# Kernel tuning notes

Measured on AMD Instinct MI355X. Metric: run time of the kernel, lower is better.

Reference implementation:

```python
import jax, jax.numpy as jnp
import numpy as np


def setup_inputs() -> dict:
    key = jax.random.key(0)
    ks = jax.random.split(key, 4)
    B, H, W, C = 4, 64, 64, 64
    d = C // 8
    s = 0.05
    return {
        "x": jax.random.normal(ks[0], (B, H, W, C), dtype=jnp.float32),
        "Wq": jax.random.normal(ks[1], (C, d), dtype=jnp.float32) * s,
        "bq": jnp.zeros((d,), dtype=jnp.float32),
        "Wk": jax.random.normal(ks[2], (C, d), dtype=jnp.float32) * s,
        "bk": jnp.zeros((d,), dtype=jnp.float32),
        "Wv": jax.random.normal(ks[3], (C, C), dtype=jnp.float32) * s,
        "bv": jnp.zeros((C,), dtype=jnp.float32),
        "gamma": jnp.zeros((1,), dtype=jnp.float32),
    }


def reference(x, Wq, bq, Wk, bk, Wv, bv, gamma):
    B, H, W, C = x.shape
    N = H * W
    xt = x.reshape(B, N, C)  # tokens = flattened spatial positions
    # 1x1 convs == per-token matmuls
    q = xt @ Wq + bq          # [B, N, C//8]
    k = xt @ Wk + bk          # [B, N, C//8]
    v = xt @ Wv + bv          # [B, N, C]
    # unscaled QK^T softmax (SAGAN uses no 1/sqrt(d) scaling)
    attn = jax.nn.softmax(jnp.einsum('bnd,bmd->bnm', q, k), axis=-1)  # [B, N, N]
    out = jnp.einsum('bnm,bmc->bnc', attn, v).reshape(B, H, W, C)
    return gamma * out + x
```

## Files before the change

### kernel.cpp

```cpp
#include <hip/hip_runtime.h>
#include <hip/hip_bf16.h>


typedef __attribute__((ext_vector_type(4))) float f32x4;

#define LOG2E 1.44269504088896340736f

#if __has_builtin(__builtin_amdgcn_exp2f)
#define EXP2(x) __builtin_amdgcn_exp2f(x)
#else
#define EXP2(x) __builtin_exp2f(x)
#endif

__device__ __forceinline__ unsigned short f2bf(float f) {
    __hip_bfloat16 h = __float2bfloat16(f);
    union { __hip_bfloat16 h; unsigned short u; } cv;
    cv.h = h;
    return cv.u;
}

__device__ __forceinline__ float bf2f(unsigned short u) {
    union { unsigned int i; float f; } cv;
    cv.i = ((unsigned int)u) << 16;
    return cv.f;
}

__global__ __launch_bounds__(256) void sagan_proj_kernel(
    const float* __restrict__ x,
    const float* __restrict__ Wq, const float* __restrict__ bq,
    const float* __restrict__ Wk, const float* __restrict__ bk,
    const float* __restrict__ Wv, const float* __restrict__ bv,
    unsigned char* __restrict__ Q8, unsigned char* __restrict__ K8,
    unsigned char* __restrict__ V8, unsigned char* __restrict__ zp)
{
    __shared__ float xs[32][68];
    const int tid = threadIdx.x;
    const int blk = blockIdx.x;
    const int tglob0 = blk << 5;
    const int b  = tglob0 >> 12;
    const int nb = tglob0 & 4095;

    if (blk == 0 && tid < 16) zp[tid] = 0;

    {
        const int t = tid >> 3, q8i = tid & 7;
        const float* src = x + (size_t)(tglob0 + t) * 64 + q8i * 8;
        *(f32x4*)&xs[t][q8i * 8]     = *(const f32x4*)(src);
        *(f32x4*)&xs[t][q8i * 8 + 4] = *(const f32x4*)(src + 4);
    }
    __syncthreads();

    {
        const int c  = tid & 63;
        const int tg = tid >> 6;
        float wcol[64];
        #pragma unroll
        for (int cc = 0; cc < 64; ++cc) wcol[cc] = Wv[cc * 64 + c];
        const float bvc = bv[c];
        float vacc[8];
        #pragma unroll
        for (int j = 0; j < 8; ++j) {
            const int tok = tg * 8 + j;
            float acc = bvc;
            #pragma unroll
            for (int c4 = 0; c4 < 16; ++c4) {
                f32x4 xv = *(const f32x4*)&xs[tok][c4 * 4];
                acc += xv[0] * wcol[c4 * 4 + 0] + xv[1] * wcol[c4 * 4 + 1]
                     + xv[2] * wcol[c4 * 4 + 2] + xv[3] * wcol[c4 * 4 + 3];
            }
            vacc[j] = acc;
        }
        int i0 = __builtin_amdgcn_cvt_pk_fp8_f32(vacc[0], vacc[1], 0, false);
        i0     = __builtin_amdgcn_cvt_pk_fp8_f32(vacc[2], vacc[3], i0, true);
        int i1 = __builtin_amdgcn_cvt_pk_fp8_f32(vacc[4], vacc[5], 0, false);
        i1     = __builtin_amdgcn_cvt_pk_fp8_f32(vacc[6], vacc[7], i1, true);
        unsigned char* dst = V8 + ((size_t)((b * 128 + (nb >> 5)) * 64 + c)) * 32
                                + tg * 8;
        *(uint2*)dst = make_uint2((unsigned int)i0, (unsigned int)i1);
    }

    if (tid < 128) {
        const int tok = tid >> 2;
        const int dp  = (tid & 3) * 2;
        float q0 = bq[dp], q1 = bq[dp + 1];
        float k0 = bk[dp], k1 = bk[dp + 1];
        #pragma unroll
        for (int cc = 0; cc < 64; ++cc) {
            const float xv = xs[tok][cc];
            const float2 wq = *(const float2*)&Wq[cc * 8 + dp];
            const float2 wk = *(const float2*)&Wk[cc * 8 + dp];
            q0 += xv * wq.x; q1 += xv * wq.y;
            k0 += xv * wk.x; k1 += xv * wk.y;
        }
        const size_t toff = (size_t)(tglob0 + tok) * 8 + dp;
        const int qi = __builtin_amdgcn_cvt_pk_fp8_f32(q0 * LOG2E, q1 * LOG2E, 0, false);
        const int ki = __builtin_amdgcn_cvt_pk_fp8_f32(k0, k1, 0, false);
        *(unsigned short*)(Q8 + toff) = (unsigned short)(qi & 0xFFFF);
        *(unsigned short*)(K8 + toff) = (unsigned short)(ki & 0xFFFF);
    }
}


#define QTILE(KA0, KA1, QF, LL, A0, A1, A2, A3, VF0, VF1, VF2, VF3) do {      \
    const f32x4 zc = {0.f, 0.f, 0.f, 0.f};                                    \
    f32x4 s0 = __builtin_amdgcn_mfma_f32_16x16x32_fp8_fp8(KA0, QF, zc, 0,0,0);\
    f32x4 s1 = __builtin_amdgcn_mfma_f32_16x16x32_fp8_fp8(KA1, QF, zc, 0,0,0);\
    float p[8];                                                               \
    _Pragma("unroll")                                                         \
    for (int r = 0; r < 4; ++r) {                                             \
        p[r]     = EXP2(s0[r]);                                               \
        p[4 + r] = EXP2(s1[r]);                                               \
    }                                                                         \
    LL += ((p[0] + p[1]) + (p[2] + p[3])) + ((p[4] + p[5]) + (p[6] + p[7]));  \
    union { int i[2]; long l; } pa;                                           \
    pa.i[0] = __builtin_amdgcn_cvt_pk_fp8_f32(p[0], p[1], 0, false);          \
    pa.i[0] = __builtin_amdgcn_cvt_pk_fp8_f32(p[2], p[3], pa.i[0], true);     \
    pa.i[1] = __builtin_amdgcn_cvt_pk_fp8_f32(p[4], p[5], 0, false);          \
    pa.i[1] = __builtin_amdgcn_cvt_pk_fp8_f32(p[6], p[7], pa.i[1], true);     \
    A0 = __builtin_amdgcn_mfma_f32_16x16x32_fp8_fp8(pa.l, VF0, A0, 0, 0, 0);  \
    A1 = __builtin_amdgcn_mfma_f32_16x16x32_fp8_fp8(pa.l, VF1, A1, 0, 0, 0);  \
    A2 = __builtin_amdgcn_mfma_f32_16x16x32_fp8_fp8(pa.l, VF2, A2, 0, 0, 0);  \
    A3 = __builtin_amdgcn_mfma_f32_16x16x32_fp8_fp8(pa.l, VF3, A3, 0, 0, 0);  \
} while (0)

__global__ __launch_bounds__(512, 4) void sagan_flash_kernel(
    const unsigned char* __restrict__ Q8, const unsigned char* __restrict__ K8,
    const unsigned char* __restrict__ V8, const unsigned char* __restrict__ zp,
    const float* __restrict__ x, const float* __restrict__ gamma_p,
    float* __restrict__ out)
{
    __shared__ unsigned short sacc[8][32][72];
    __shared__ float sl[8][32];

    const int tid  = threadIdx.x;
    const int lane = tid & 63;
    const int w    = tid >> 6;
    const int g    = lane >> 4;
    const int ql   = lane & 15;
    const int blk  = blockIdx.x;
    const int b    = blk >> 7;
    const int qbase = (blk & 127) << 5;

    const unsigned char* Kbase = K8 + (size_t)b * (4096 * 8);
    const unsigned char* Qbase = Q8 + (size_t)b * (4096 * 8);

    long qf0, qf1;
    {
        const unsigned char* qp = Qbase + (size_t)(qbase + ql) * 8;
        qf0 = (g == 0) ? *(const long*)(qp)       : 0L;
        qf1 = (g == 0) ? *(const long*)(qp + 128) : 0L;
    }

    const int kt0 = w << 9;

    const unsigned char* kp0;
    int kstep;
    if (g == 0) {
        const int kperm = ((ql >> 2) << 3) | (ql & 3);
        kp0 = Kbase + (size_t)(kt0 + kperm) * 8;
        kstep = 256;
    } else {
        kp0 = zp; kstep = 0;
    }

    const unsigned char* vp = V8 + (size_t)(b * 128 + w * 16) * 2048
                                 + ql * 32 + g * 8;

    f32x4 acc00 = {0.f,0.f,0.f,0.f}, acc01 = acc00, acc02 = acc00, acc03 = acc00;
    f32x4 acc10 = acc00, acc11 = acc00, acc12 = acc00, acc13 = acc00;
    float l0 = 0.f, l1 = 0.f;

    #pragma unroll 1
    for (int it = 0; it < 16; ++it) {
        const long ka0 = *(const long*)kp0;
        const long ka1 = *(const long*)(kp0 + 32);
        kp0 += kstep;
        const long vf0 = *(const long*)(vp);
        const long vf1 = *(const long*)(vp + 512);
        const long vf2 = *(const long*)(vp + 1024);
        const long vf3 = *(const long*)(vp + 1536);
        vp += 2048;

        __builtin_amdgcn_s_setprio(1);
        QTILE(ka0, ka1, qf0, l0, acc00, acc01, acc02, acc03, vf0, vf1, vf2, vf3);
        QTILE(ka0, ka1, qf1, l1, acc10, acc11, acc12, acc13, vf0, vf1, vf2, vf3);
        __builtin_amdgcn_s_setprio(0);
    }

    l0 += __shfl_xor(l0, 16); l0 += __shfl_xor(l0, 32);
    l1 += __shfl_xor(l1, 16); l1 += __shfl_xor(l1, 32);

    #pragma unroll
    for (int r = 0; r < 4; ++r) {
        const int row = (g << 2) | r;
        unsigned short* d0 = &sacc[w][row][0];
        d0[ql] = f2bf(acc00[r]); d0[16 + ql] = f2bf(acc01[r]);
        d0[32 + ql] = f2bf(acc02[r]); d0[48 + ql] = f2bf(acc03[r]);
        unsigned short* d1 = &sacc[w][16 + row][0];
        d1[ql] = f2bf(acc10[r]); d1[16 + ql] = f2bf(acc11[r]);
        d1[32 + ql] = f2bf(acc12[r]); d1[48 + ql] = f2bf(acc13[r]);
    }
    if (g == 0) {
        sl[w][ql] = l0; sl[w][16 + ql] = l1;
    }
    __syncthreads();

    {
        const int row = tid >> 4;
        const int c4  = tid & 15;
        float L = 0.f;
        float O[4] = {0.f, 0.f, 0.f, 0.f};
        #pragma unroll
        for (int ww = 0; ww < 8; ++ww) {
            L += sl[ww][row];
            const uint2 v = *(const uint2*)&sacc[ww][row][c4 * 4];
            O[0] += bf2f((unsigned short)(v.x & 0xFFFF));
            O[1] += bf2f((unsigned short)(v.x >> 16));
            O[2] += bf2f((unsigned short)(v.y & 0xFFFF));
            O[3] += bf2f((unsigned short)(v.y >> 16));
        }
        const float Li = 1.0f / L;
        const float gm = gamma_p[0];
        const size_t off = ((size_t)(b * 4096 + qbase + row)) * 64 + c4 * 4;
        const f32x4 xv = *(const f32x4*)(x + off);
        f32x4 o;
        o[0] = gm * (O[0] * Li) + xv[0];
        o[1] = gm * (O[1] * Li) + xv[1];
        o[2] = gm * (O[2] * Li) + xv[2];
        o[3] = gm * (O[3] * Li) + xv[3];
        *(f32x4*)(out + off) = o;
    }
}

extern "C" void kernel_launch(void* const* d_in, const int* in_sizes, int n_in,
                              void* d_out, int out_size, void* d_ws, size_t ws_size,
                              hipStream_t stream) {
    const float* x  = (const float*)d_in[0];
    const float* Wq = (const float*)d_in[1];
    const float* bq = (const float*)d_in[2];
    const float* Wk = (const float*)d_in[3];
    const float* bk = (const float*)d_in[4];
    const float* Wv = (const float*)d_in[5];
    const float* bv = (const float*)d_in[6];
    const float* gm = (const float*)d_in[7];
    float* out = (float*)d_out;

    unsigned char* Q8 = (unsigned char*)d_ws;
    unsigned char* K8 = Q8 + 131072;
    unsigned char* V8 = K8 + 131072;
    unsigned char* zp = V8 + 1048576;

    hipLaunchKernelGGL(sagan_proj_kernel, dim3(512), dim3(256), 0, stream,
                       x, Wq, bq, Wk, bk, Wv, bv, Q8, K8, V8, zp);
    hipLaunchKernelGGL(sagan_flash_kernel, dim3(512), dim3(512), 0, stream,
                       Q8, K8, V8, zp, x, gm, out);
}
```

Baseline: 30.10 us.

## Compute QKV projections with bf16 MFMA and use cheap bf16 rounding

```diff
diff --git a/kernel.cpp b/kernel.cpp
--- a/kernel.cpp
+++ b/kernel.cpp
@@ -3,6 +3,7 @@
 
 
 typedef __attribute__((ext_vector_type(4))) float f32x4;
+typedef __attribute__((ext_vector_type(8))) short short8;
 
 #define LOG2E 1.44269504088896340736f
 
@@ -12,17 +13,22 @@
 #define EXP2(x) __builtin_exp2f(x)
 #endif
 
-__device__ __forceinline__ unsigned short f2bf(float f) {
-    __hip_bfloat16 h = __float2bfloat16(f);
-    union { __hip_bfloat16 h; unsigned short u; } cv;
-    cv.h = h;
-    return cv.u;
-}
-
 __device__ __forceinline__ float bf2f(unsigned short u) {
     union { unsigned int i; float f; } cv;
     cv.i = ((unsigned int)u) << 16;
     return cv.f;
+}
+
+__device__ __forceinline__ unsigned int pkbf_rnd(float lo, float hi) {
+    union { float f; unsigned int u; } a, b;
+    a.f = lo; b.f = hi;
+    const unsigned int ar = a.u + 0x8000u;
+    const unsigned int br = b.u + 0x8000u;
+    return __builtin_amdgcn_perm(br, ar, 0x07060302u);
+}
+
+__device__ __forceinline__ unsigned char f2fp8(float v) {
+    return (unsigned char)(__builtin_amdgcn_cvt_pk_fp8_f32(v, v, 0, false) & 0xFF);
 }
 
 __global__ __launch_bounds__(256) void sagan_proj_kernel(
@@ -33,70 +39,85 @@
     unsigned char* __restrict__ Q8, unsigned char* __restrict__ K8,
     unsigned char* __restrict__ V8, unsigned char* __restrict__ zp)
 {
-    __shared__ float xs[32][68];
-    const int tid = threadIdx.x;
-    const int blk = blockIdx.x;
+    const int tid  = threadIdx.x;
+    const int lane = tid & 63;
+    const int w    = tid >> 6;
+    const int g    = lane >> 4;
+    const int ql   = lane & 15;
+    const int blk  = blockIdx.x;
     const int tglob0 = blk << 5;
-    const int b  = tglob0 >> 12;
-    const int nb = tglob0 & 4095;
+    const int b    = tglob0 >> 12;
+    const int nb   = tglob0 & 4095;
+    const int chunk = nb >> 5;
 
     if (blk == 0 && tid < 16) zp[tid] = 0;
 
+    short8 xa[2][2];
+    #pragma unroll
+    for (int t = 0; t < 2; ++t) {
+        const float* xr = x + (size_t)(tglob0 + t * 16 + ql) * 64 + g * 8;
+        #pragma unroll
+        for (int s = 0; s < 2; ++s) {
+            const f32x4 lo = *(const f32x4*)(xr + s * 32);
+            const f32x4 hi = *(const f32x4*)(xr + s * 32 + 4);
+            union { unsigned int u[4]; short8 v; } pk;
+            pk.u[0] = pkbf_rnd(lo[0], lo[1]);
+            pk.u[1] = pkbf_rnd(lo[2], lo[3]);
+            pk.u[2] = pkbf_rnd(hi[0], hi[1]);
+            pk.u[3] = pkbf_rnd(hi[2], hi[3]);
+            xa[t][s] = pk.v;
+        }
+    }
+
+    const f32x4 zc = {0.f, 0.f, 0.f, 0.f};
+
     {
-        const int t = tid >> 3, q8i = tid & 7;
-        const float* src = x + (size_t)(tglob0 + t) * 64 + q8i * 8;
-        *(f32x4*)&xs[t][q8i * 8]     = *(const f32x4*)(src);
-        *(f32x4*)&xs[t][q8i * 8 + 4] = *(const f32x4*)(src + 4);
-    }
-    __syncthreads();
-
-    {
-        const int c  = tid & 63;
-        const int tg = tid >> 6;
-        float wcol[64];
-        #pragma unroll
-        for (int cc = 0; cc < 64; ++cc) wcol[cc] = Wv[cc * 64 + c];
-        const float bvc = bv[c];
-        float vacc[8];
-        #pragma unroll
-        for (int j = 0; j < 8; ++j) {
-            const int tok = tg * 8 + j;
-            float acc = bvc;
+        const int cp = w * 16 + ql;
+        short8 bf[2];
+        #pragma unroll
+        for (int s = 0; s < 2; ++s) {
+            const float* wp = Wv + (size_t)(s * 32 + g * 8) * 64 + cp;
+            union { unsigned int u[4]; short8 v; } pk;
             #pragma unroll
-            for (int c4 = 0; c4 < 16; ++c4) {
-                f32x4 xv = *(const f32x4*)&xs[tok][c4 * 4];
-                acc += xv[0] * wcol[c4 * 4 + 0] + xv[1] * wcol[c4 * 4 + 1]
-                     + xv[2] * wcol[c4 * 4 + 2] + xv[3] * wcol[c4 * 4 + 3];
-            }
-            vacc[j] = acc;
-        }
-        int i0 = __builtin_amdgcn_cvt_pk_fp8_f32(vacc[0], vacc[1], 0, false);
-        i0     = __builtin_amdgcn_cvt_pk_fp8_f32(vacc[2], vacc[3], i0, true);
-        int i1 = __builtin_amdgcn_cvt_pk_fp8_f32(vacc[4], vacc[5], 0, false);
-        i1     = __builtin_amdgcn_cvt_pk_fp8_f32(vacc[6], vacc[7], i1, true);
-        unsigned char* dst = V8 + ((size_t)((b * 128 + (nb >> 5)) * 64 + c)) * 32
-                                + tg * 8;
-        *(uint2*)dst = make_uint2((unsigned int)i0, (unsigned int)i1);
-    }
-
-    if (tid < 128) {
-        const int tok = tid >> 2;
-        const int dp  = (tid & 3) * 2;
-        float q0 = bq[dp], q1 = bq[dp + 1];
-        float k0 = bk[dp], k1 = bk[dp + 1];
-        #pragma unroll
-        for (int cc = 0; cc < 64; ++cc) {
-            const float xv = xs[tok][cc];
-            const float2 wq = *(const float2*)&Wq[cc * 8 + dp];
-            const float2 wk = *(const float2*)&Wk[cc * 8 + dp];
-            q0 += xv * wq.x; q1 += xv * wq.y;
-            k0 += xv * wk.x; k1 += xv * wk.y;
-        }
-        const size_t toff = (size_t)(tglob0 + tok) * 8 + dp;
-        const int qi = __builtin_amdgcn_cvt_pk_fp8_f32(q0 * LOG2E, q1 * LOG2E, 0, false);
-        const int ki = __builtin_amdgcn_cvt_pk_fp8_f32(k0, k1, 0, false);
-        *(unsigned short*)(Q8 + toff) = (unsigned short)(qi & 0xFFFF);
-        *(unsigned short*)(K8 + toff) = (unsigned short)(ki & 0xFFFF);
+            for (int jj = 0; jj < 4; ++jj)
+                pk.u[jj] = pkbf_rnd(wp[(jj * 2) * 64], wp[(jj * 2 + 1) * 64]);
+            bf[s] = pk.v;
+        }
+        const float bvc = bv[cp];
+        #pragma unroll
+        for (int t = 0; t < 2; ++t) {
+            f32x4 acc = __builtin_amdgcn_mfma_f32_16x16x32_bf16(xa[t][0], bf[0], zc, 0, 0, 0);
+            acc = __builtin_amdgcn_mfma_f32_16x16x32_bf16(xa[t][1], bf[1], acc, 0, 0, 0);
+            int pk8 = __builtin_amdgcn_cvt_pk_fp8_f32(acc[0] + bvc, acc[1] + bvc, 0, false);
+            pk8     = __builtin_amdgcn_cvt_pk_fp8_f32(acc[2] + bvc, acc[3] + bvc, pk8, true);
+            unsigned char* dst = V8 + ((size_t)((b * 128 + chunk) * 64 + cp)) * 32
+                                    + t * 16 + g * 4;
+            *(unsigned int*)dst = (unsigned int)pk8;
+        }
+    }
+
+    if (w < 2) {
+        short8 bqk[2];
+        const bool isQ = (ql < 8);
+        const int dcol = isQ ? ql : (ql - 8);
+        #pragma unroll
+        for (int s = 0; s < 2; ++s) {
+            const float* wp = (isQ ? Wq : Wk) + (size_t)(s * 32 + g * 8) * 8 + dcol;
+            const float sc = isQ ? LOG2E : 1.0f;
+            union { unsigned int u[4]; short8 v; } pk;
+            #pragma unroll
+            for (int jj = 0; jj < 4; ++jj)
+                pk.u[jj] = pkbf_rnd(wp[(jj * 2) * 8] * sc, wp[(jj * 2 + 1) * 8] * sc);
+            bqk[s] = pk.v;
+        }
+        const float bias = isQ ? (bq[dcol] * LOG2E) : bk[dcol];
+        f32x4 acc = __builtin_amdgcn_mfma_f32_16x16x32_bf16(xa[w][0], bqk[0], zc, 0, 0, 0);
+        acc = __builtin_amdgcn_mfma_f32_16x16x32_bf16(xa[w][1], bqk[1], acc, 0, 0, 0);
+        unsigned char* base = (isQ ? Q8 : K8)
+                            + (size_t)(tglob0 + w * 16 + g * 4) * 8 + dcol;
+        #pragma unroll
+        for (int r = 0; r < 4; ++r)
+            base[r * 8] = f2fp8(acc[r] + bias);
     }
 }
 
@@ -194,11 +215,15 @@
     for (int r = 0; r < 4; ++r) {
         const int row = (g << 2) | r;
         unsigned short* d0 = &sacc[w][row][0];
-        d0[ql] = f2bf(acc00[r]); d0[16 + ql] = f2bf(acc01[r]);
-        d0[32 + ql] = f2bf(acc02[r]); d0[48 + ql] = f2bf(acc03[r]);
+        d0[ql] = (unsigned short)(pkbf_rnd(acc00[r], acc00[r]) & 0xFFFF);
+        d0[16 + ql] = (unsigned short)(pkbf_rnd(acc01[r], acc01[r]) & 0xFFFF);
+        d0[32 + ql] = (unsigned short)(pkbf_rnd(acc02[r], acc02[r]) & 0xFFFF);
+        d0[48 + ql] = (unsigned short)(pkbf_rnd(acc03[r], acc03[r]) & 0xFFFF);
         unsigned short* d1 = &sacc[w][16 + row][0];
-        d1[ql] = f2bf(acc10[r]); d1[16 + ql] = f2bf(acc11[r]);
-        d1[32 + ql] = f2bf(acc12[r]); d1[48 + ql] = f2bf(acc13[r]);
+        d1[ql] = (unsigned short)(pkbf_rnd(acc10[r], acc10[r]) & 0xFFFF);
+        d1[16 + ql] = (unsigned short)(pkbf_rnd(acc11[r], acc11[r]) & 0xFFFF);
+        d1[32 + ql] = (unsigned short)(pkbf_rnd(acc12[r], acc12[r]) & 0xFFFF);
+        d1[48 + ql] = (unsigned short)(pkbf_rnd(acc13[r], acc13[r]) & 0xFFFF);
     }
     if (g == 0) {
         sl[w][ql] = l0; sl[w][16 + ql] = l1;
```

Result: faster. 29.06 us (-3.4%).
